# Kernel optimization log

Hardware: AMD Instinct MI355X
Metric: run time of the kernel (lower is better)

The kernel has to match this reference:

```python
import jax, jax.numpy as jnp
import numpy as np

B, C, T, E = 8, 64, 128, 256
TYPE_NUM, NF = 40, 128
KS = (5, 4, 3)
NEG = -1e10


def setup_inputs() -> dict:
    key = jax.random.key(0)
    ks = jax.random.split(key, 10)
    s = 0.02
    return {
        "query": jax.random.normal(ks[0], (C, E), jnp.float32),
        "context": jax.random.normal(ks[1], (B, T, E), jnp.float32),
        "mask": jax.random.randint(ks[2], (B, T), 0, 2, jnp.int32),
        "W_hidden": jax.random.normal(ks[3], (4 * E, 4 * E), jnp.float32) * s,
        "b_hidden": jnp.zeros((4 * E,), jnp.float32),
        "W_v": jax.random.normal(ks[4], (1, 4 * E), jnp.float32) * s,
        "b_v": jnp.zeros((1,), jnp.float32),
        "W_lin": jax.random.normal(ks[5], (E, 4 * E), jnp.float32) * s,
        "b_lin": jnp.zeros((E,), jnp.float32),
        "conv_w0": jax.random.normal(ks[6], (NF, E, KS[0]), jnp.float32) * s,
        "conv_b0": jnp.zeros((NF,), jnp.float32),
        "conv_w1": jax.random.normal(ks[7], (NF, E, KS[1]), jnp.float32) * s,
        "conv_b1": jnp.zeros((NF,), jnp.float32),
        "conv_w2": jax.random.normal(ks[8], (NF, E, KS[2]), jnp.float32) * s,
        "conv_b2": jnp.zeros((NF,), jnp.float32),
        "W_cnn": jax.random.normal(ks[9], (TYPE_NUM, NF * 3), jnp.float32) * s,
        "b_cnn": jnp.zeros((TYPE_NUM,), jnp.float32),
    }


def _pair_feat(a, b):
    # [.., e] x2 -> [.., 4e]: [a, b, |a-b|, a*b]
    return jnp.concatenate([a, b, jnp.abs(a - b), a * b], axis=-1)


def _conv1d(x, w, b):
    # x: [b, e, c], w: [f, e, k] (torch Conv1d layout) -> [b, f, c-k+1]
    y = jax.lax.conv_general_dilated(
        x, w, window_strides=(1,), padding="VALID",
        dimension_numbers=("NCH", "OIH", "NCH"))
    return y + b[None, :, None]


def reference(query, context, mask, W_hidden, b_hidden, W_v, b_v,
              W_lin, b_lin, conv_w0, conv_b0, conv_w1, conv_b1,
              conv_w2, conv_b2, W_cnn, b_cnn):
    b, t, e = context.shape
    c = query.shape[0]
    q_ = jnp.broadcast_to(query[None, :, None, :], (b, c, t, e))
    ctx_ = jnp.broadcast_to(context[:, None, :, :], (b, c, t, e))
    feat = _pair_feat(q_, ctx_)                                 # [b,c,t,4e]
    h = jnp.tanh(feat @ W_hidden.T + b_hidden)                  # [b,c,t,4e]
    scores = (h @ W_v.T + b_v)[..., 0]                          # [b,c,t]
    scores = jnp.where((mask < 1)[:, None, :], NEG, scores)
    attn = jax.nn.softmax(scores, axis=-1)                      # [b,c,t]
    g = jnp.einsum("bct,bte->bce", attn, context)               # [b,c,e]
    q2 = jnp.broadcast_to(query[None], (b, c, e))
    h2 = jnp.tanh(_pair_feat(q2, g) @ W_hidden.T + b_hidden)    # [b,c,4e]
    x = h2 @ W_lin.T + b_lin                                    # [b,c,e]
    xT = jnp.transpose(x, (0, 2, 1))                            # [b,e,c]
    pooled = []
    for w, bb in ((conv_w0, conv_b0), (conv_w1, conv_b1), (conv_w2, conv_b2)):
        y = jax.nn.relu(_conv1d(xT, w, bb))                     # [b,f,c-k+1]
        pooled.append(jnp.max(y, axis=2))                       # [b,f]
    cnn = jnp.concatenate(pooled, axis=1)                       # [b,3f]
    return cnn @ W_cnn.T + b_cnn                                # [b,type_num]
```

## Files before the change

### kernel.cpp

```cpp
#include <hip/hip_runtime.h>
#include <math.h>


typedef __bf16 bf16x8 __attribute__((ext_vector_type(8)));
typedef float  f32x4  __attribute__((ext_vector_type(4)));

__device__ __forceinline__ float ftanh(float v) {
    float t = __expf(2.f * v);
    return 1.f - 2.f * __builtin_amdgcn_rcpf(t + 1.f);
}

__device__ __forceinline__ void gld_lds16(const __bf16* g, __bf16* l) {
    __builtin_amdgcn_global_load_lds(
        (const __attribute__((address_space(1))) void*)g,
        (__attribute__((address_space(3))) void*)l, 16, 0, 0);
}

__global__ __launch_bounds__(256) void gemm_tn_kernel(
    const float* __restrict__ A, int lda,
    const float* __restrict__ B, int ldb,
    const float* __restrict__ bias,
    float* __restrict__ C, int ldc, int K)
{
    __shared__ float As[16][68];
    __shared__ float Bs[16][68];
    const int tid = threadIdx.x;
    const int m0 = blockIdx.y * 64, n0 = blockIdx.x * 64;
    const int tm = tid >> 4, tn = tid & 15;
    const int lr = tid >> 2;
    const int lc = (tid & 3) * 4;

    float acc[4][4];
#pragma unroll
    for (int i = 0; i < 4; ++i)
#pragma unroll
        for (int j = 0; j < 4; ++j) acc[i][j] = 0.f;

    for (int k0 = 0; k0 < K; k0 += 16) {
        float4 av = *reinterpret_cast<const float4*>(A + (size_t)(m0 + lr) * lda + k0 + lc);
        float4 bv = *reinterpret_cast<const float4*>(B + (size_t)(n0 + lr) * ldb + k0 + lc);
        As[lc + 0][lr] = av.x; As[lc + 1][lr] = av.y; As[lc + 2][lr] = av.z; As[lc + 3][lr] = av.w;
        Bs[lc + 0][lr] = bv.x; Bs[lc + 1][lr] = bv.y; Bs[lc + 2][lr] = bv.z; Bs[lc + 3][lr] = bv.w;
        __syncthreads();
#pragma unroll
        for (int kk = 0; kk < 16; ++kk) {
            float4 a = *reinterpret_cast<const float4*>(&As[kk][tm * 4]);
            float4 b = *reinterpret_cast<const float4*>(&Bs[kk][tn * 4]);
            float ar[4] = {a.x, a.y, a.z, a.w};
            float br[4] = {b.x, b.y, b.z, b.w};
#pragma unroll
            for (int i = 0; i < 4; ++i)
#pragma unroll
                for (int j = 0; j < 4; ++j) acc[i][j] += ar[i] * br[j];
        }
        __syncthreads();
    }

#pragma unroll
    for (int i = 0; i < 4; ++i) {
        int m = m0 + tm * 4 + i;
        float vals[4];
#pragma unroll
        for (int j = 0; j < 4; ++j) {
            int n = n0 + tn * 4 + j;
            vals[j] = acc[i][j] + (bias ? bias[n] : 0.f);
        }
        float4 o; o.x = vals[0]; o.y = vals[1]; o.z = vals[2]; o.w = vals[3];
        *reinterpret_cast<float4*>(C + (size_t)m * ldc + n0 + tn * 4) = o;
    }
}

__global__ void cvt_kernel(const float* __restrict__ Wh, const float* __restrict__ Wl,
                           const float* __restrict__ ctx,
                           const float* __restrict__ cw0, const float* __restrict__ cw1,
                           const float* __restrict__ cw2,
                           __bf16* __restrict__ Whbf, __bf16* __restrict__ Whbf_t,
                           __bf16* __restrict__ Wlbf, __bf16* __restrict__ ctxbf,
                           float* __restrict__ wt0, float* __restrict__ wt1,
                           float* __restrict__ wt2, float* __restrict__ gsc)
{
    int idx = blockIdx.x * 256 + threadIdx.x;
    if (idx < 1048576) { Whbf[idx] = (__bf16)Wh[idx]; return; }
    if (idx < 1114112) {
        int di = idx - 1048576;
        int ng = di >> 13, kc = (di >> 10) & 7;
        int row = (di >> 3) & 127, kgp = di & 7;
        int kg = kgp ^ (row & 7);
        const float* s = Wh + (size_t)(ng * 128 + row) * 1024 + 512 + kc * 64 + kg * 8;
        bf16x8 u;
#pragma unroll
        for (int i = 0; i < 8; ++i) u[i] = (__bf16)s[i];
        *reinterpret_cast<bf16x8*>(Whbf_t + (size_t)di * 8) = u;
        return;
    }
    if (idx < 1376256) { int j = idx - 1114112; Wlbf[j] = (__bf16)Wl[j]; return; }
    if (idx < 1409024) {
        int di = idx - 1376256;
        const float* s = ctx + (size_t)di * 8;
        bf16x8 u;
#pragma unroll
        for (int i = 0; i < 8; ++i) u[i] = (__bf16)s[i];
        *reinterpret_cast<bf16x8*>(ctxbf + (size_t)di * 8) = u;
        return;
    }
    if (idx < 1572864) {
        int j = idx - 1409024; int f = j & 127, rest = j >> 7;
        int i = rest % 5, e = rest / 5;
        wt0[j] = cw0[(size_t)(f * 256 + e) * 5 + i]; return;
    }
    if (idx < 1703936) {
        int j = idx - 1572864; int f = j & 127, rest = j >> 7;
        int i = rest & 3, e = rest >> 2;
        wt1[j] = cw1[(size_t)(f * 256 + e) * 4 + i]; return;
    }
    if (idx < 1802240) {
        int j = idx - 1703936; int f = j & 127, rest = j >> 7;
        int i = rest % 3, e = rest / 3;
        wt2[j] = cw2[(size_t)(f * 256 + e) * 3 + i]; return;
    }
    gsc[idx - 1802240] = 0.f;
}

__global__ __launch_bounds__(512, 4) void attn_mfma_kernel(
    const float* __restrict__ q,
    const float* __restrict__ ctx,
    const __bf16* __restrict__ Whbf_t,
    const float* __restrict__ Wv,
    const float* __restrict__ Apre,
    const float* __restrict__ Bpre,
    float* __restrict__ gsc)
{
    __shared__ __bf16 Us[256 * 64];
    __shared__ __bf16 Ws[128 * 64];
    __shared__ float qc[512];
    __shared__ float sc[256];

    const int tid = threadIdx.x;
    const int cpair = blockIdx.x >> 3, ng = blockIdx.x & 7;
    const int b = cpair >> 5, c0 = (cpair & 31) * 2;
    const int wave = tid >> 6, lane = tid & 63;
    const int w1 = wave & 1, w0 = wave >> 1;
    const int m0 = w0 * 64;
    const int l15 = lane & 15, quad = lane >> 4;
    const int swz = l15 & 7;
    const int kg = tid & 7;

    qc[tid] = q[(size_t)(c0 + (tid >> 8)) * 256 + (tid & 255)];
    if (tid < 256) sc[tid] = 0.f;
    __syncthreads();

    f32x4 acc[4][4];
#pragma unroll
    for (int mi = 0; mi < 4; ++mi)
#pragma unroll
        for (int ni = 0; ni < 4; ++ni) acc[mi][ni] = (f32x4){0.f, 0.f, 0.f, 0.f};

    for (int kc = 0; kc < 8; ++kc) {
        const bool isabs = (kc < 4);
        const int e0 = (kc & 3) * 64;
        const int eb = e0 + kg * 8;
        float qA[8], qB[8];
#pragma unroll
        for (int i = 0; i < 8; ++i) { qA[i] = qc[eb + i]; qB[i] = qc[256 + eb + i]; }
        bf16x8 u0[2], u1[2];
#pragma unroll
        for (int it = 0; it < 2; ++it) {
            const int trow = it * 64 + (tid >> 3);
            const float* cp = ctx + (size_t)(b * 128 + trow) * 256 + eb;
            float4 cl0 = *reinterpret_cast<const float4*>(cp);
            float4 cl1 = *reinterpret_cast<const float4*>(cp + 4);
            float cv[8] = {cl0.x, cl0.y, cl0.z, cl0.w, cl1.x, cl1.y, cl1.z, cl1.w};
#pragma unroll
            for (int i = 0; i < 8; ++i) {
                u0[it][i] = (__bf16)(isabs ? fabsf(qA[i] - cv[i]) : qA[i] * cv[i]);
                u1[it][i] = (__bf16)(isabs ? fabsf(qB[i] - cv[i]) : qB[i] * cv[i]);
            }
        }
        __syncthreads();
        const __bf16* wtile = Whbf_t + (size_t)(ng * 8 + kc) * 8192;
#pragma unroll
        for (int it = 0; it < 2; ++it) {
            int gidx = wave * 128 + it * 64;
            gld_lds16(wtile + (size_t)(gidx + lane) * 8, &Ws[gidx * 8]);
        }
#pragma unroll
        for (int it = 0; it < 2; ++it) {
            const int trow = it * 64 + (tid >> 3);
            const int off = (kg ^ (trow & 7)) * 8;
            *reinterpret_cast<bf16x8*>(&Us[trow * 64 + off]) = u0[it];
            *reinterpret_cast<bf16x8*>(&Us[(trow + 128) * 64 + off]) = u1[it];
        }
        __syncthreads();
#pragma unroll
        for (int ks = 0; ks < 2; ++ks) {
            const int c8 = (((ks * 4 + quad) ^ swz)) * 8;
            bf16x8 a[4], bfr[4];
#pragma unroll
            for (int mi = 0; mi < 4; ++mi)
                a[mi] = *reinterpret_cast<const bf16x8*>(
                    &Us[(m0 + mi * 16 + l15) * 64 + c8]);
#pragma unroll
            for (int ni = 0; ni < 4; ++ni)
                bfr[ni] = *reinterpret_cast<const bf16x8*>(
                    &Ws[(w1 * 64 + ni * 16 + l15) * 64 + c8]);
#pragma unroll
            for (int mi = 0; mi < 4; ++mi)
#pragma unroll
                for (int ni = 0; ni < 4; ++ni)
                    acc[mi][ni] = __builtin_amdgcn_mfma_f32_16x16x32_bf16(
                        a[mi], bfr[ni], acc[mi][ni], 0, 0, 0);
        }
    }

    const int jcol = ng * 128 + w1 * 64 + l15;
    const int c = c0 + (w0 >> 1);
    float av[4], wv[4];
#pragma unroll
    for (int ni = 0; ni < 4; ++ni) {
        av[ni] = Apre[(size_t)c * 1024 + jcol + ni * 16];
        wv[ni] = Wv[jcol + ni * 16];
    }
#pragma unroll
    for (int mi = 0; mi < 4; ++mi) {
        const int tb = (w0 & 1) * 64 + mi * 16 + quad * 4;
        float p[4];
#pragma unroll
        for (int r = 0; r < 4; ++r) {
            const float* bp = Bpre + (size_t)(b * 128 + tb + r) * 1024 + jcol;
            float s = 0.f;
#pragma unroll
            for (int ni = 0; ni < 4; ++ni)
                s += ftanh(acc[mi][ni][r] + av[ni] + bp[ni * 16]) * wv[ni];
            p[r] = s;
        }
#pragma unroll
        for (int off = 1; off < 16; off <<= 1)
#pragma unroll
            for (int r = 0; r < 4; ++r) p[r] += __shfl_xor(p[r], off, 16);
        if (l15 == 0) {
#pragma unroll
            for (int r = 0; r < 4; ++r)
                atomicAdd(&sc[(w0 >> 1) * 128 + tb + r], p[r]);
        }
    }
    __syncthreads();

    if (tid < 256) atomicAdd(&gsc[(size_t)(b * 64 + c0) * 128 + tid], sc[tid]);
}

__global__ __launch_bounds__(256) void attn_tail_kernel(
    const float* __restrict__ ctx, const int* __restrict__ mask,
    const float* __restrict__ bv, const float* __restrict__ gsc,
    float* __restrict__ g)
{
    __shared__ float sc[128];
    __shared__ float red;
    const int tid = threadIdx.x;
    const int bc = blockIdx.x, b = bc >> 6;

    if (tid < 128) {
        float s = gsc[(size_t)bc * 128 + tid] + bv[0];
        if (mask[b * 128 + tid] < 1) s = -1e10f;
        sc[tid] = s;
    }
    __syncthreads();
    if (tid < 64) {
        float m = fmaxf(sc[tid], sc[tid + 64]);
        for (int off = 32; off; off >>= 1) m = fmaxf(m, __shfl_xor(m, off, 64));
        if (tid == 0) red = m;
    }
    __syncthreads();
    const float mx = red;
    if (tid < 128) sc[tid] = __expf(sc[tid] - mx);
    __syncthreads();
    if (tid < 64) {
        float s = sc[tid] + sc[tid + 64];
        for (int off = 32; off; off >>= 1) s += __shfl_xor(s, off, 64);
        if (tid == 0) red = s;
    }
    __syncthreads();
    const float inv = 1.f / red;

    float gv = 0.f;
    for (int t = 0; t < 128; ++t) gv += sc[t] * ctx[(size_t)(b * 128 + t) * 256 + tid];
    g[(size_t)bc * 256 + tid] = gv * inv;
}

__global__ void feat2_kernel(const float* __restrict__ q, const float* __restrict__ g,
                             __bf16* __restrict__ feat2)
{
    int row = blockIdx.x, e = threadIdx.x;
    int c = row & 63;
    float qv = q[c * 256 + e], gv = g[row * 256 + e];
    __bf16* o = feat2 + (size_t)row * 768 + e;
    o[0]   = (__bf16)gv;
    o[256] = (__bf16)fabsf(qv - gv);
    o[512] = (__bf16)(qv * gv);
}

template <int ACT, int OUTBF, int BMODE>
__global__ __launch_bounds__(256) void mfma_gemm_kernel(
    const __bf16* __restrict__ A, int lda,
    const __bf16* __restrict__ B, int ldb,
    const float* __restrict__ bias, void* __restrict__ Cout,
    int K, int ldc)
{
    __shared__ __bf16 As[64 * 72];
    __shared__ __bf16 Bs[64 * 72];
    const int tid = threadIdx.x;
    const int wave = tid >> 6, lane = tid & 63;
    const int w0 = wave >> 1, w1 = wave & 1;
    const int l15 = lane & 15, quad = lane >> 4;
    const int m0 = blockIdx.y * 64, n0 = blockIdx.x * 64;

    f32x4 acc[2][2];
#pragma unroll
    for (int mi = 0; mi < 2; ++mi)
#pragma unroll
        for (int ni = 0; ni < 2; ++ni) acc[mi][ni] = (f32x4){0.f, 0.f, 0.f, 0.f};

    for (int k0 = 0; k0 < K; k0 += 64) {
        __syncthreads();
#pragma unroll
        for (int it = 0; it < 2; ++it) {
            int idx = tid + it * 256;
            int row = idx >> 3, kgi = idx & 7;
            int4 va = *reinterpret_cast<const int4*>(A + (size_t)(m0 + row) * lda + k0 + kgi * 8);
            *reinterpret_cast<int4*>(&As[row * 72 + kgi * 8]) = va;
            int4 vb = *reinterpret_cast<const int4*>(B + (size_t)(n0 + row) * ldb + k0 + kgi * 8);
            *reinterpret_cast<int4*>(&Bs[row * 72 + kgi * 8]) = vb;
        }
        __syncthreads();
#pragma unroll
        for (int ks = 0; ks < 2; ++ks) {
            bf16x8 a[2], bb[2];
#pragma unroll
            for (int mi = 0; mi < 2; ++mi)
                a[mi] = *reinterpret_cast<const bf16x8*>(
                    &As[(w0 * 32 + mi * 16 + l15) * 72 + ks * 32 + quad * 8]);
#pragma unroll
            for (int ni = 0; ni < 2; ++ni)
                bb[ni] = *reinterpret_cast<const bf16x8*>(
                    &Bs[(w1 * 32 + ni * 16 + l15) * 72 + ks * 32 + quad * 8]);
#pragma unroll
            for (int mi = 0; mi < 2; ++mi)
#pragma unroll
                for (int ni = 0; ni < 2; ++ni)
                    acc[mi][ni] = __builtin_amdgcn_mfma_f32_16x16x32_bf16(
                        a[mi], bb[ni], acc[mi][ni], 0, 0, 0);
        }
    }

#pragma unroll
    for (int mi = 0; mi < 2; ++mi)
#pragma unroll
        for (int ni = 0; ni < 2; ++ni) {
            int col = n0 + w1 * 32 + ni * 16 + l15;
#pragma unroll
            for (int r = 0; r < 4; ++r) {
                int row = m0 + w0 * 32 + mi * 16 + quad * 4 + r;
                float bsv = (BMODE == 0) ? bias[col]
                          : (BMODE == 1) ? bias[(row & 63) * 1024 + col] : 0.f;
                float v = acc[mi][ni][r] + bsv;
                if (ACT) v = ftanh(v);
                if (OUTBF) ((__bf16*)Cout)[(size_t)row * ldc + col] = (__bf16)v;
                else       ((float*)Cout)[(size_t)row * ldc + col] = v;
            }
        }
}

template <int KW>
__device__ __forceinline__ void conv_body(
    const float* __restrict__ x, const float* __restrict__ wt,
    float* __restrict__ part, int b, int chunk, int bi, float* xs)
{
    const int tid = threadIdx.x;
    const int f = tid & 127, esub = tid >> 7;
    const int e0 = chunk * 64;

#pragma unroll
    for (int it = 0; it < 16; ++it) {
        int idx = tid + it * 256;
        int e = idx & 63, p = idx >> 6;
        xs[e * 72 + p] = x[(size_t)(b * 64 + p) * 256 + e0 + e];
    }
    __syncthreads();

    float acc[64];
#pragma unroll
    for (int p = 0; p < 64; ++p) acc[p] = 0.f;

    for (int ei = 0; ei < 32; ++ei) {
        const int eL = esub * 32 + ei;
        float wreg[KW];
#pragma unroll
        for (int i = 0; i < KW; ++i)
            wreg[i] = wt[(size_t)((e0 + eL) * KW + i) * 128 + f];
        float xv[68];
#pragma unroll
        for (int k4 = 0; k4 < 17; ++k4) {
            float4 v = *reinterpret_cast<const float4*>(&xs[eL * 72 + k4 * 4]);
            xv[k4 * 4 + 0] = v.x; xv[k4 * 4 + 1] = v.y;
            xv[k4 * 4 + 2] = v.z; xv[k4 * 4 + 3] = v.w;
        }
#pragma unroll
        for (int i = 0; i < KW; ++i)
#pragma unroll
            for (int p = 0; p < 64; ++p)
                acc[p] = fmaf(wreg[i], xv[p + i], acc[p]);
    }

    float* op = part + ((size_t)(bi * 2 + esub)) * 8192 + f;
#pragma unroll
    for (int p = 0; p < 64; ++p) op[p * 128] = acc[p];
}

__global__ __launch_bounds__(256) void conv_partial_kernel(
    const float* __restrict__ x,
    const float* __restrict__ wt0, const float* __restrict__ wt1,
    const float* __restrict__ wt2, float* __restrict__ part)
{
    __shared__ float xs[64 * 72];
    const int bi = blockIdx.x;
    const int kw = bi >> 5, b = (bi >> 2) & 7, chunk = bi & 3;
    if (kw == 0)      conv_body<5>(x, wt0, part, b, chunk, bi, xs);
    else if (kw == 1) conv_body<4>(x, wt1, part, b, chunk, bi, xs);
    else              conv_body<3>(x, wt2, part, b, chunk, bi, xs);
}

__global__ __launch_bounds__(128) void reduce_pool_kernel(
    const float* __restrict__ part,
    const float* __restrict__ b0, const float* __restrict__ b1,
    const float* __restrict__ b2, float* __restrict__ cnn)
{
    const int bi = blockIdx.x;
    const int kw = bi >> 3, b = bi & 7;
    const int f = threadIdx.x;
    const int KW = 5 - kw, P = 64 - KW + 1;
    const float bias = (kw == 0 ? b0 : kw == 1 ? b1 : b2)[f];
    float mx = 0.f;
    for (int p = 0; p < P; ++p) {
        float s = 0.f;
#pragma unroll
        for (int c4 = 0; c4 < 4; ++c4)
#pragma unroll
            for (int es = 0; es < 2; ++es)
                s += part[((size_t)((kw * 32 + b * 4 + c4) * 2 + es)) * 8192 + p * 128 + f];
        s += bias;
        mx = fmaxf(mx, s);
    }
    cnn[b * 384 + kw * 128 + f] = mx;
}

__global__ void final_kernel(const float* __restrict__ cnn, const float* __restrict__ Wc,
                             const float* __restrict__ bc, float* __restrict__ out)
{
    int o = threadIdx.x;
    if (o >= 320) return;
    int b = o / 40, t = o - b * 40;
    float s = bc[t];
    for (int i = 0; i < 384; ++i) s += cnn[b * 384 + i] * Wc[t * 384 + i];
    out[o] = s;
}

extern "C" void kernel_launch(void* const* d_in, const int* in_sizes, int n_in,
                              void* d_out, int out_size, void* d_ws, size_t ws_size,
                              hipStream_t stream)
{
    (void)in_sizes; (void)n_in; (void)out_size; (void)ws_size;
    const float* q    = (const float*)d_in[0];
    const float* ctx  = (const float*)d_in[1];
    const int*   mask = (const int*)d_in[2];
    const float* Wh   = (const float*)d_in[3];
    const float* bh   = (const float*)d_in[4];
    const float* Wv   = (const float*)d_in[5];
    const float* bv   = (const float*)d_in[6];
    const float* Wl   = (const float*)d_in[7];
    const float* bl   = (const float*)d_in[8];
    const float* cw0  = (const float*)d_in[9];
    const float* cb0  = (const float*)d_in[10];
    const float* cw1  = (const float*)d_in[11];
    const float* cb1  = (const float*)d_in[12];
    const float* cw2  = (const float*)d_in[13];
    const float* cb2  = (const float*)d_in[14];
    const float* Wc   = (const float*)d_in[15];
    const float* bc   = (const float*)d_in[16];

    float* ws   = (float*)d_ws;
    float* Apre = ws;
    float* g    = Apre + 65536;
    float* x    = g + 131072;
    float* cnn  = x + 131072;
    float* part = cnn + 3072;
    float* wt0  = part + 1572864;
    float* wt1  = wt0 + 163840;
    float* wt2  = wt1 + 131072;
    __bf16* bfb    = (__bf16*)(wt2 + 98304);
    __bf16* Whbf   = bfb;
    __bf16* Wlbf   = bfb + 1048576;
    __bf16* feat2b = bfb + 1310720;
    __bf16* h2b    = bfb + 1703936;
    float*  gsc    = (float*)(bfb + 2228224);
    __bf16* Whbf_t = (__bf16*)part;
    __bf16* ctxbf  = Whbf_t + 524288;
    float*  Bpre   = (float*)(ctxbf + 262144);

    dim3 blk(256);
    cvt_kernel<<<7296, blk, 0, stream>>>(Wh, Wl, ctx, cw0, cw1, cw2,
                                         Whbf, Whbf_t, Wlbf, ctxbf, wt0, wt1, wt2, gsc);
    gemm_tn_kernel<<<dim3(16, 1), blk, 0, stream>>>(q, 256, Wh, 1024, bh, Apre, 1024, 256);
    mfma_gemm_kernel<0, 0, 2><<<dim3(16, 16), blk, 0, stream>>>(
        ctxbf, 256, Whbf + 256, 1024, nullptr, Bpre, 256, 1024);
    attn_mfma_kernel<<<2048, dim3(512), 0, stream>>>(q, ctx, Whbf_t, Wv, Apre, Bpre, gsc);
    attn_tail_kernel<<<512, blk, 0, stream>>>(ctx, mask, bv, gsc, g);
    feat2_kernel<<<512, blk, 0, stream>>>(q, g, feat2b);
    mfma_gemm_kernel<1, 1, 1><<<dim3(16, 8), blk, 0, stream>>>(
        feat2b, 768, Whbf + 256, 1024, Apre, h2b, 768, 1024);
    mfma_gemm_kernel<0, 0, 0><<<dim3(4, 8), blk, 0, stream>>>(
        h2b, 1024, Wlbf, 1024, bl, x, 1024, 256);
    conv_partial_kernel<<<96, blk, 0, stream>>>(x, wt0, wt1, wt2, part);
    reduce_pool_kernel<<<24, 128, 0, stream>>>(part, cb0, cb1, cb2, cnn);
    final_kernel<<<1, 320, 0, stream>>>(cnn, Wc, bc, (float*)d_out);
}
```

Before: 321.0 us.

## Retile attention MFMA kernel to one query per block and fuse feat2 into tail

The attention MFMA kernel now gives each block one (b,c) pair with a 128x256 output tile instead of two queries over a 256x128 tile. Each block loads a larger W tile, and the pre-transposed weight layout is regrouped into 256-row groups to match. The feat2 construction is folded into the softmax tail kernel, which removes one launch and the round trip of g through global memory. The retile trades less A-side work per block for more W loads into LDS per block; grid size stays the same.

```diff
diff --git a/kernel.cpp b/kernel.cpp
--- a/kernel.cpp
+++ b/kernel.cpp
@@ -83,10 +83,10 @@
     if (idx < 1048576) { Whbf[idx] = (__bf16)Wh[idx]; return; }
     if (idx < 1114112) {
         int di = idx - 1048576;
-        int ng = di >> 13, kc = (di >> 10) & 7;
-        int row = (di >> 3) & 127, kgp = di & 7;
+        int ng = di >> 14, kc = (di >> 11) & 7;
+        int row = (di >> 3) & 255, kgp = di & 7;
         int kg = kgp ^ (row & 7);
-        const float* s = Wh + (size_t)(ng * 128 + row) * 1024 + 512 + kc * 64 + kg * 8;
+        const float* s = Wh + (size_t)(ng * 256 + row) * 1024 + 512 + kc * 64 + kg * 8;
         bf16x8 u;
 #pragma unroll
         for (int i = 0; i < 8; ++i) u[i] = (__bf16)s[i];
@@ -130,23 +130,23 @@
     const float* __restrict__ Bpre,
     float* __restrict__ gsc)
 {
-    __shared__ __bf16 Us[256 * 64];
-    __shared__ __bf16 Ws[128 * 64];
-    __shared__ float qc[512];
-    __shared__ float sc[256];
+    __shared__ __bf16 Us[128 * 64];
+    __shared__ __bf16 Ws[256 * 64];
+    __shared__ float qc[256];
+    __shared__ float sc[128];
 
     const int tid = threadIdx.x;
-    const int cpair = blockIdx.x >> 3, ng = blockIdx.x & 7;
-    const int b = cpair >> 5, c0 = (cpair & 31) * 2;
+    const int bc = blockIdx.x >> 2, ng = blockIdx.x & 3;
+    const int b = bc >> 6, c = bc & 63;
     const int wave = tid >> 6, lane = tid & 63;
-    const int w1 = wave & 1, w0 = wave >> 1;
-    const int m0 = w0 * 64;
+    const int wm = wave >> 2, wn = wave & 3;
+    const int m0 = wm * 64;
     const int l15 = lane & 15, quad = lane >> 4;
     const int swz = l15 & 7;
     const int kg = tid & 7;
 
-    qc[tid] = q[(size_t)(c0 + (tid >> 8)) * 256 + (tid & 255)];
-    if (tid < 256) sc[tid] = 0.f;
+    if (tid < 256) qc[tid] = q[(size_t)c * 256 + tid];
+    if (tid < 128) sc[tid] = 0.f;
     __syncthreads();
 
     f32x4 acc[4][4];
@@ -159,36 +159,32 @@
         const bool isabs = (kc < 4);
         const int e0 = (kc & 3) * 64;
         const int eb = e0 + kg * 8;
-        float qA[8], qB[8];
-#pragma unroll
-        for (int i = 0; i < 8; ++i) { qA[i] = qc[eb + i]; qB[i] = qc[256 + eb + i]; }
-        bf16x8 u0[2], u1[2];
+        float qv8[8];
+#pragma unroll
+        for (int i = 0; i < 8; ++i) qv8[i] = qc[eb + i];
+        bf16x8 u[2];
 #pragma unroll
         for (int it = 0; it < 2; ++it) {
-            const int trow = it * 64 + (tid >> 3);
+            const int trow = (tid + it * 512) >> 3;
             const float* cp = ctx + (size_t)(b * 128 + trow) * 256 + eb;
             float4 cl0 = *reinterpret_cast<const float4*>(cp);
             float4 cl1 = *reinterpret_cast<const float4*>(cp + 4);
             float cv[8] = {cl0.x, cl0.y, cl0.z, cl0.w, cl1.x, cl1.y, cl1.z, cl1.w};
 #pragma unroll
-            for (int i = 0; i < 8; ++i) {
-                u0[it][i] = (__bf16)(isabs ? fabsf(qA[i] - cv[i]) : qA[i] * cv[i]);
-                u1[it][i] = (__bf16)(isabs ? fabsf(qB[i] - cv[i]) : qB[i] * cv[i]);
-            }
+            for (int i = 0; i < 8; ++i)
+                u[it][i] = (__bf16)(isabs ? fabsf(qv8[i] - cv[i]) : qv8[i] * cv[i]);
         }
         __syncthreads();
-        const __bf16* wtile = Whbf_t + (size_t)(ng * 8 + kc) * 8192;
+        const __bf16* wtile = Whbf_t + (size_t)(ng * 8 + kc) * 16384;
+#pragma unroll
+        for (int it = 0; it < 4; ++it) {
+            int gidx = wave * 256 + it * 64;
+            gld_lds16(wtile + (size_t)(gidx + lane) * 8, &Ws[gidx * 8]);
+        }
 #pragma unroll
         for (int it = 0; it < 2; ++it) {
-            int gidx = wave * 128 + it * 64;
-            gld_lds16(wtile + (size_t)(gidx + lane) * 8, &Ws[gidx * 8]);
-        }
-#pragma unroll
-        for (int it = 0; it < 2; ++it) {
-            const int trow = it * 64 + (tid >> 3);
-            const int off = (kg ^ (trow & 7)) * 8;
-            *reinterpret_cast<bf16x8*>(&Us[trow * 64 + off]) = u0[it];
-            *reinterpret_cast<bf16x8*>(&Us[(trow + 128) * 64 + off]) = u1[it];
+            const int trow = (tid + it * 512) >> 3;
+            *reinterpret_cast<bf16x8*>(&Us[trow * 64 + (kg ^ (trow & 7)) * 8]) = u[it];
         }
         __syncthreads();
 #pragma unroll
@@ -202,7 +198,7 @@
 #pragma unroll
             for (int ni = 0; ni < 4; ++ni)
                 bfr[ni] = *reinterpret_cast<const bf16x8*>(
-                    &Ws[(w1 * 64 + ni * 16 + l15) * 64 + c8]);
+                    &Ws[(wn * 64 + ni * 16 + l15) * 64 + c8]);
 #pragma unroll
             for (int mi = 0; mi < 4; ++mi)
 #pragma unroll
@@ -212,8 +208,7 @@
         }
     }
 
-    const int jcol = ng * 128 + w1 * 64 + l15;
-    const int c = c0 + (w0 >> 1);
+    const int jcol = ng * 256 + wn * 64 + l15;
     float av[4], wv[4];
 #pragma unroll
     for (int ni = 0; ni < 4; ++ni) {
@@ -222,7 +217,7 @@
     }
 #pragma unroll
     for (int mi = 0; mi < 4; ++mi) {
-        const int tb = (w0 & 1) * 64 + mi * 16 + quad * 4;
+        const int tb = m0 + mi * 16 + quad * 4;
         float p[4];
 #pragma unroll
         for (int r = 0; r < 4; ++r) {
@@ -240,23 +235,23 @@
         if (l15 == 0) {
 #pragma unroll
             for (int r = 0; r < 4; ++r)
-                atomicAdd(&sc[(w0 >> 1) * 128 + tb + r], p[r]);
-        }
-    }
-    __syncthreads();
-
-    if (tid < 256) atomicAdd(&gsc[(size_t)(b * 64 + c0) * 128 + tid], sc[tid]);
+                atomicAdd(&sc[tb + r], p[r]);
+        }
+    }
+    __syncthreads();
+
+    if (tid < 128) atomicAdd(&gsc[(size_t)bc * 128 + tid], sc[tid]);
 }
 
 __global__ __launch_bounds__(256) void attn_tail_kernel(
     const float* __restrict__ ctx, const int* __restrict__ mask,
     const float* __restrict__ bv, const float* __restrict__ gsc,
-    float* __restrict__ g)
+    const float* __restrict__ q, __bf16* __restrict__ feat2)
 {
     __shared__ float sc[128];
     __shared__ float red;
     const int tid = threadIdx.x;
-    const int bc = blockIdx.x, b = bc >> 6;
+    const int bc = blockIdx.x, b = bc >> 6, c = bc & 63;
 
     if (tid < 128) {
         float s = gsc[(size_t)bc * 128 + tid] + bv[0];
@@ -283,16 +278,9 @@
 
     float gv = 0.f;
     for (int t = 0; t < 128; ++t) gv += sc[t] * ctx[(size_t)(b * 128 + t) * 256 + tid];
-    g[(size_t)bc * 256 + tid] = gv * inv;
-}
-
-__global__ void feat2_kernel(const float* __restrict__ q, const float* __restrict__ g,
-                             __bf16* __restrict__ feat2)
-{
-    int row = blockIdx.x, e = threadIdx.x;
-    int c = row & 63;
-    float qv = q[c * 256 + e], gv = g[row * 256 + e];
-    __bf16* o = feat2 + (size_t)row * 768 + e;
+    gv *= inv;
+    const float qv = q[(size_t)c * 256 + tid];
+    __bf16* o = feat2 + (size_t)bc * 768 + tid;
     o[0]   = (__bf16)gv;
     o[256] = (__bf16)fabsf(qv - gv);
     o[512] = (__bf16)(qv * gv);
@@ -512,8 +500,7 @@
     mfma_gemm_kernel<0, 0, 2><<<dim3(16, 16), blk, 0, stream>>>(
         ctxbf, 256, Whbf + 256, 1024, nullptr, Bpre, 256, 1024);
     attn_mfma_kernel<<<2048, dim3(512), 0, stream>>>(q, ctx, Whbf_t, Wv, Apre, Bpre, gsc);
-    attn_tail_kernel<<<512, blk, 0, stream>>>(ctx, mask, bv, gsc, g);
-    feat2_kernel<<<512, blk, 0, stream>>>(q, g, feat2b);
+    attn_tail_kernel<<<512, blk, 0, stream>>>(ctx, mask, bv, gsc, q, feat2b);
     mfma_gemm_kernel<1, 1, 1><<<dim3(16, 8), blk, 0, stream>>>(
         feat2b, 768, Whbf + 256, 1024, Apre, h2b, 768, 1024);
     mfma_gemm_kernel<0, 0, 0><<<dim3(4, 8), blk, 0, stream>>>(
```

Result: slower. 412.2 us (+28.4%).
